# Kernel tuning notes

Measured on AMD Instinct MI355X. Metric: run time of the kernel, lower is better.

Reference implementation:

```python
import jax, jax.numpy as jnp
import numpy as np

NEG_SLOPE = 0.2


def _build_dense_adj(edge_list, n):
    # edge_list: [2, E] int; symmetric 0/1 dense adjacency like edge_list_to_dense
    a = jnp.zeros((n, n), jnp.float32)
    a = a.at[edge_list[0], edge_list[1]].set(1.0)
    a = a.at[edge_list[1], edge_list[0]].set(1.0)
    return a


def setup_inputs() -> dict:
    key = jax.random.key(0)
    k1, k2, k3, k4 = jax.random.split(key, 4)
    N, T, D, H, E = 4096, 3, 16, 4, 65536
    scores = jax.random.normal(k1, (N, 1), jnp.float32)
    edge_type_emb = jax.random.normal(k2, (T, D), jnp.float32)
    att_w = jax.random.normal(k3, (H, D + 2, 1), jnp.float32) * 0.1  # xavier-ish
    edge_list = jax.random.randint(k4, (T, 2, E), 0, N, jnp.int64)
    return {"scores": scores, "edge_type_emb": edge_type_emb,
            "att_w": att_w, "edge_list": edge_list}


def reference(scores, edge_type_emb, att_w, edge_list):
    # scores: [N,1]; edge_type_emb: [T,D]; att_w: [H,D+2,1]; edge_list: [T,2,E]
    N = scores.shape[0]
    adjs = jax.vmap(lambda el: _build_dense_adj(el, N))(edge_list)  # [T,N,N]
    sum_adj = adjs.sum(axis=0)  # [N,N]
    s = scores[:, 0]            # [N]

    def head(w):
        w = w[:, 0]
        w_src, w_mid, w_tgt = w[0], w[1:-1], w[-1]
        # per-edge-type scalar from edge embedding dotted with middle weights
        c = edge_type_emb @ w_mid                    # [T]
        edge_term = jnp.einsum('tij,t->ij', adjs, c)  # [N,N]
        # (i,j): adj*(w_src*s_i) + adj*edge_emb.w_mid + adj*(w_tgt*s_j)
        logits = sum_adj * (w_src * s[:, None] + w_tgt * s[None, :]) + edge_term
        logits = jnp.where(logits >= 0, logits, NEG_SLOPE * logits)  # LeakyReLU
        att = jax.nn.softmax(logits, axis=-1)  # dense row softmax (as original)
        return att @ scores  # [N,1]

    outs = jax.vmap(head)(att_w)  # [H,N,1]
    return outs.mean(axis=0)      # average over heads
```

## Files before the change

### kernel.cpp

```cpp
#include <hip/hip_runtime.h>

#define NEG_SLOPE_F 0.2f

static constexpr int Nn = 4096;
static constexpr int Tt = 3;
static constexpr int Dd = 16;
static constexpr int Hh = 4;
static constexpr int CAP = 256;
static constexpr int WPR = 128;

__device__ __forceinline__ float waveMax(float v) {
#pragma unroll
  for (int m = 1; m < 64; m <<= 1) v = fmaxf(v, __shfl_xor(v, m));
  return v;
}
__device__ __forceinline__ float waveSum(float v) {
#pragma unroll
  for (int m = 1; m < 64; m <<= 1) v += __shfl_xor(v, m);
  return v;
}

__global__ void prep_kernel(const float* __restrict__ scores,
                            const float* __restrict__ emb,
                            const float* __restrict__ attw,
                            float* __restrict__ pv) {
  __shared__ float rb[4];
  int tid = threadIdx.x;
  float s = 0.f;
  for (int j = tid; j < Nn; j += 256) s += scores[j];
  s = waveSum(s);
  if ((tid & 63) == 0) rb[tid >> 6] = s;
  __syncthreads();
  if (tid == 0) pv[12] = rb[0] + rb[1] + rb[2] + rb[3];
  if (tid < Hh * Tt) {
    int h = tid / Tt, t = tid % Tt;
    float c = 0.f;
#pragma unroll
    for (int d = 0; d < Dd; ++d) c += emb[t * Dd + d] * attw[h * (Dd + 2) + 1 + d];
    pv[tid] = c;
  }
}

__global__ void or_kernel(const int* __restrict__ el,
                          unsigned int* __restrict__ bitmap, int E) {
  int e = blockIdx.x * blockDim.x + threadIdx.x;
  if (e >= E) return;
  int t = blockIdx.y;
  int dir = blockIdx.z;
  unsigned int a = (unsigned int)el[(t * 2 + dir) * E + e];
  unsigned int b = (unsigned int)el[(t * 2 + (1 - dir)) * E + e];
  atomicOr(&bitmap[(a * 3u + t) * WPR + (b >> 5)], 1u << (b & 31u));
}

__launch_bounds__(256)
__global__ void compact_kernel(const unsigned int* __restrict__ bitmap,
                               unsigned short* __restrict__ list,
                               unsigned int* __restrict__ cnt) {
  int wid = threadIdx.x >> 6, lane = threadIdx.x & 63;
  int row = blockIdx.x * 4 + wid;
  const unsigned int* bm = bitmap + (size_t)row * 3 * WPR;
  unsigned int w[2][3];
#pragma unroll
  for (int p = 0; p < 2; ++p)
#pragma unroll
    for (int t = 0; t < 3; ++t) w[p][t] = bm[t * WPR + p * 64 + lane];
  unsigned int orw[2];
  orw[0] = w[0][0] | w[0][1] | w[0][2];
  orw[1] = w[1][0] | w[1][1] | w[1][2];
  int c = __popc(orw[0]) + __popc(orw[1]);
  int off = c;
#pragma unroll
  for (int d = 1; d < 64; d <<= 1) {
    int tv = __shfl_up(off, d);
    if (lane >= d) off += tv;
  }
  int total = __shfl(off, 63);
  off -= c;
  if (lane == 0) cnt[row] = (unsigned int)(total < CAP ? total : CAP);
  unsigned short* dst = list + (size_t)row * CAP;
  int idx = off;
#pragma unroll
  for (int p = 0; p < 2; ++p) {
    unsigned int o = orw[p];
    int jbase = (p * 64 + lane) * 32;
    while (o) {
      int b = __ffs(o) - 1;
      o &= o - 1;
      unsigned int m = ((w[p][0] >> b) & 1u) | (((w[p][1] >> b) & 1u) << 1) |
                       (((w[p][2] >> b) & 1u) << 2);
      if (idx < CAP) dst[idx] = (unsigned short)((jbase + b) | (m << 12));
      ++idx;
    }
  }
}

__launch_bounds__(256)
__global__ void row_kernel(const unsigned short* __restrict__ list,
                           const unsigned int* __restrict__ cnt,
                           const float* __restrict__ scores,
                           const float* __restrict__ attw,
                           const float* __restrict__ pv,
                           float* __restrict__ out) {
  int wid = threadIdx.x >> 6, lane = threadIdx.x & 63;
  int i = blockIdx.x * 4 + wid;
  int n = (int)cnt[i];
  float si = scores[i];
  float wsrc[Hh], wtgt[Hh], c0[Hh], c1[Hh], c2[Hh];
#pragma unroll
  for (int h = 0; h < Hh; ++h) {
    wsrc[h] = attw[h * (Dd + 2) + 0];
    wtgt[h] = attw[h * (Dd + 2) + Dd + 1];
    c0[h] = pv[h * 3 + 0];
    c1[h] = pv[h * 3 + 1];
    c2[h] = pv[h * 3 + 2];
  }
  float Ssum = pv[12];

  constexpr int IT = CAP / 64;
  float lv[IT][Hh], sjv[IT];
  float mx[Hh];
#pragma unroll
  for (int h = 0; h < Hh; ++h) mx[h] = -INFINITY;
  float sedge = 0.f;

#pragma unroll
  for (int it = 0; it < IT; ++it) {
    if (it * 64 >= n) break;
    int k = it * 64 + lane;
    bool act = k < n;
    unsigned int v = act ? (unsigned int)list[(size_t)i * CAP + k] : 0u;
    int j = (int)(v & 0xFFFu);
    int m = act ? (int)(v >> 12) : 0;
    float sj = act ? scores[j] : 0.f;
    sjv[it] = sj;
    if (act) sedge += sj;
    float na = (float)__popc(m);
    float et0 = (m & 1) ? 1.f : 0.f;
    float et1 = (m & 2) ? 1.f : 0.f;
    float et2 = (m & 4) ? 1.f : 0.f;
#pragma unroll
    for (int h = 0; h < Hh; ++h) {
      float et = et0 * c0[h] + et1 * c1[h] + et2 * c2[h];
      float l = na * (wsrc[h] * si + wtgt[h] * sj) + et;
      l = (l >= 0.f) ? l : NEG_SLOPE_F * l;
      lv[it][h] = act ? l : -INFINITY;
      mx[h] = fmaxf(mx[h], lv[it][h]);
    }
  }

#pragma unroll
  for (int h = 0; h < Hh; ++h) {
    mx[h] = waveMax(mx[h]);
    if (n < Nn) mx[h] = fmaxf(mx[h], 0.f);
  }

  float se[Hh], ss[Hh];
#pragma unroll
  for (int h = 0; h < Hh; ++h) { se[h] = 0.f; ss[h] = 0.f; }
#pragma unroll
  for (int it = 0; it < IT; ++it) {
    if (it * 64 >= n) break;
#pragma unroll
    for (int h = 0; h < Hh; ++h) {
      float ex = expf(lv[it][h] - mx[h]);
      se[h] += ex;
      ss[h] += ex * sjv[it];
    }
  }
  sedge = waveSum(sedge);
#pragma unroll
  for (int h = 0; h < Hh; ++h) {
    se[h] = waveSum(se[h]);
    ss[h] = waveSum(ss[h]);
  }
  if (lane == 0) {
    float acc = 0.f;
#pragma unroll
    for (int h = 0; h < Hh; ++h) {
      float nz = expf(-mx[h]);
      float denom = se[h] + nz * ((float)Nn - (float)n);
      float numer = ss[h] + nz * (Ssum - sedge);
      acc += numer / denom;
    }
    out[i] = acc * (1.f / (float)Hh);
  }
}

extern "C" void kernel_launch(void* const* d_in, const int* in_sizes, int n_in,
                              void* d_out, int out_size, void* d_ws, size_t ws_size,
                              hipStream_t stream) {
  const float* scores = (const float*)d_in[0];
  const float* emb    = (const float*)d_in[1];
  const float* attw   = (const float*)d_in[2];
  const int*   el     = (const int*)d_in[3];
  float* out = (float*)d_out;
  int E = in_sizes[3] / (Tt * 2);

  size_t bm_bytes = (size_t)Nn * 3 * WPR * 4;
  unsigned int* bitmap = (unsigned int*)d_ws;
  unsigned int* cnt = (unsigned int*)((char*)d_ws + bm_bytes);
  float* pv = (float*)((char*)cnt + Nn * sizeof(unsigned int));
  unsigned short* list = (unsigned short*)((char*)pv + 64);

  hipMemsetAsync(d_ws, 0, bm_bytes + Nn * sizeof(unsigned int), stream);
  prep_kernel<<<1, 256, 0, stream>>>(scores, emb, attw, pv);
  or_kernel<<<dim3((E + 255) / 256, Tt, 2), 256, 0, stream>>>(el, bitmap, E);
  compact_kernel<<<Nn / 4, 256, 0, stream>>>(bitmap, list, cnt);
  row_kernel<<<Nn / 4, 256, 0, stream>>>(list, cnt, scores, attw, pv, out);
}
```

Before: 40.92 us.

## Fuse compaction into row kernel and merge bitmap clear with prep

Replaces the memset and single-block prep launch with one grid-stride kernel that zeroes the bitmap and, in block 0, computes the score sum and per-head edge constants. The compaction stage now runs inside the row kernel and writes neighbor lists to shared memory instead of global memory, which drops the global list and count buffers and one kernel launch. The OR kernel handles both edge directions in one thread instead of two grid slices. The cost is a larger row kernel with a shared-memory staging buffer and a block barrier.

```diff
diff --git a/kernel.cpp b/kernel.cpp
--- a/kernel.cpp
+++ b/kernel.cpp
@@ -20,24 +20,32 @@
   return v;
 }
 
-__global__ void prep_kernel(const float* __restrict__ scores,
-                            const float* __restrict__ emb,
-                            const float* __restrict__ attw,
-                            float* __restrict__ pv) {
-  __shared__ float rb[4];
-  int tid = threadIdx.x;
-  float s = 0.f;
-  for (int j = tid; j < Nn; j += 256) s += scores[j];
-  s = waveSum(s);
-  if ((tid & 63) == 0) rb[tid >> 6] = s;
-  __syncthreads();
-  if (tid == 0) pv[12] = rb[0] + rb[1] + rb[2] + rb[3];
-  if (tid < Hh * Tt) {
-    int h = tid / Tt, t = tid % Tt;
-    float c = 0.f;
-#pragma unroll
-    for (int d = 0; d < Dd; ++d) c += emb[t * Dd + d] * attw[h * (Dd + 2) + 1 + d];
-    pv[tid] = c;
+__global__ void clear_prep_kernel(uint4* __restrict__ bm4,
+                                  const float* __restrict__ scores,
+                                  const float* __restrict__ emb,
+                                  const float* __restrict__ attw,
+                                  float* __restrict__ pv) {
+  const int total = Nn * 3 * WPR / 4;
+  uint4 z = make_uint4(0u, 0u, 0u, 0u);
+  for (int k = blockIdx.x * 256 + threadIdx.x; k < total; k += gridDim.x * 256)
+    bm4[k] = z;
+  if (blockIdx.x == 0) {
+    __shared__ float rb[4];
+    int tid = threadIdx.x;
+    float s = 0.f;
+    for (int j = tid; j < Nn; j += 256) s += scores[j];
+    s = waveSum(s);
+    if ((tid & 63) == 0) rb[tid >> 6] = s;
+    __syncthreads();
+    if (tid == 0) pv[12] = rb[0] + rb[1] + rb[2] + rb[3];
+    if (tid < Hh * Tt) {
+      int h = tid / Tt, t = tid % Tt;
+      float c = 0.f;
+#pragma unroll
+      for (int d = 0; d < Dd; ++d)
+        c += emb[t * Dd + d] * attw[h * (Dd + 2) + 1 + d];
+      pv[tid] = c;
+    }
   }
 }
 
@@ -46,19 +54,23 @@
   int e = blockIdx.x * blockDim.x + threadIdx.x;
   if (e >= E) return;
   int t = blockIdx.y;
-  int dir = blockIdx.z;
-  unsigned int a = (unsigned int)el[(t * 2 + dir) * E + e];
-  unsigned int b = (unsigned int)el[(t * 2 + (1 - dir)) * E + e];
+  unsigned int a = (unsigned int)el[(t * 2 + 0) * E + e];
+  unsigned int b = (unsigned int)el[(t * 2 + 1) * E + e];
   atomicOr(&bitmap[(a * 3u + t) * WPR + (b >> 5)], 1u << (b & 31u));
+  atomicOr(&bitmap[(b * 3u + t) * WPR + (a >> 5)], 1u << (a & 31u));
 }
 
 __launch_bounds__(256)
-__global__ void compact_kernel(const unsigned int* __restrict__ bitmap,
-                               unsigned short* __restrict__ list,
-                               unsigned int* __restrict__ cnt) {
+__global__ void row_kernel(const unsigned int* __restrict__ bitmap,
+                           const float* __restrict__ scores,
+                           const float* __restrict__ attw,
+                           const float* __restrict__ pv,
+                           float* __restrict__ out) {
+  __shared__ unsigned short lst[4][CAP];
   int wid = threadIdx.x >> 6, lane = threadIdx.x & 63;
-  int row = blockIdx.x * 4 + wid;
-  const unsigned int* bm = bitmap + (size_t)row * 3 * WPR;
+  int i = blockIdx.x * 4 + wid;
+  const unsigned int* bm = bitmap + (size_t)i * 3 * WPR;
+
   unsigned int w[2][3];
 #pragma unroll
   for (int p = 0; p < 2; ++p)
@@ -74,10 +86,9 @@
     int tv = __shfl_up(off, d);
     if (lane >= d) off += tv;
   }
-  int total = __shfl(off, 63);
+  int n = __shfl(off, 63);
   off -= c;
-  if (lane == 0) cnt[row] = (unsigned int)(total < CAP ? total : CAP);
-  unsigned short* dst = list + (size_t)row * CAP;
+  if (n > CAP) n = CAP;
   int idx = off;
 #pragma unroll
   for (int p = 0; p < 2; ++p) {
@@ -88,22 +99,12 @@
       o &= o - 1;
       unsigned int m = ((w[p][0] >> b) & 1u) | (((w[p][1] >> b) & 1u) << 1) |
                        (((w[p][2] >> b) & 1u) << 2);
-      if (idx < CAP) dst[idx] = (unsigned short)((jbase + b) | (m << 12));
+      if (idx < CAP) lst[wid][idx] = (unsigned short)((jbase + b) | (m << 12));
       ++idx;
     }
   }
-}
-
-__launch_bounds__(256)
-__global__ void row_kernel(const unsigned short* __restrict__ list,
-                           const unsigned int* __restrict__ cnt,
-                           const float* __restrict__ scores,
-                           const float* __restrict__ attw,
-                           const float* __restrict__ pv,
-                           float* __restrict__ out) {
-  int wid = threadIdx.x >> 6, lane = threadIdx.x & 63;
-  int i = blockIdx.x * 4 + wid;
-  int n = (int)cnt[i];
+  __syncthreads();
+
   float si = scores[i];
   float wsrc[Hh], wtgt[Hh], c0[Hh], c1[Hh], c2[Hh];
 #pragma unroll
@@ -128,7 +129,7 @@
     if (it * 64 >= n) break;
     int k = it * 64 + lane;
     bool act = k < n;
-    unsigned int v = act ? (unsigned int)list[(size_t)i * CAP + k] : 0u;
+    unsigned int v = act ? (unsigned int)lst[wid][k] : 0u;
     int j = (int)(v & 0xFFFu);
     int m = act ? (int)(v >> 12) : 0;
     float sj = act ? scores[j] : 0.f;
@@ -198,13 +199,9 @@
 
   size_t bm_bytes = (size_t)Nn * 3 * WPR * 4;
   unsigned int* bitmap = (unsigned int*)d_ws;
-  unsigned int* cnt = (unsigned int*)((char*)d_ws + bm_bytes);
-  float* pv = (float*)((char*)cnt + Nn * sizeof(unsigned int));
-  unsigned short* list = (unsigned short*)((char*)pv + 64);
-
-  hipMemsetAsync(d_ws, 0, bm_bytes + Nn * sizeof(unsigned int), stream);
-  prep_kernel<<<1, 256, 0, stream>>>(scores, emb, attw, pv);
-  or_kernel<<<dim3((E + 255) / 256, Tt, 2), 256, 0, stream>>>(el, bitmap, E);
-  compact_kernel<<<Nn / 4, 256, 0, stream>>>(bitmap, list, cnt);
-  row_kernel<<<Nn / 4, 256, 0, stream>>>(list, cnt, scores, attw, pv, out);
-}
+  float* pv = (float*)((char*)d_ws + bm_bytes);
+
+  clear_prep_kernel<<<768, 256, 0, stream>>>((uint4*)d_ws, scores, emb, attw, pv);
+  or_kernel<<<dim3((E + 255) / 256, Tt), 256, 0, stream>>>(el, bitmap, E);
+  row_kernel<<<Nn / 4, 256, 0, stream>>>(bitmap, scores, attw, pv, out);
+}
```

Result: faster. 35.66 us (-12.9%).
